# Optimization experiments

Measured on AMD Instinct MI355X. Metric: run time of the kernel, lower is better.

The kernel has to match this reference:

```python
import jax, jax.numpy as jnp
from jax import lax
import numpy as np

N_E = 1024
E_DIM = 512
BETA = 0.25


def setup_inputs() -> dict:
    key = jax.random.key(0)
    k1, k2 = jax.random.split(key)
    z = jax.random.normal(k1, (16, 4096, E_DIM), dtype=jnp.float32)
    # torch init: uniform(-1/n_e, 1/n_e)
    codebook = jax.random.uniform(k2, (N_E, E_DIM), dtype=jnp.float32,
                                  minval=-1.0 / N_E, maxval=1.0 / N_E)
    return {"z": z, "codebook": codebook}


def reference(z, codebook):
    zf = z.reshape(-1, z.shape[-1])                      # (N, e_dim)
    # squared-distance matrix: ||z||^2 + ||e||^2 - 2 z e^T  -> (N, n_e)
    d = (jnp.sum(zf * zf, axis=1, keepdims=True)
         + jnp.sum(codebook * codebook, axis=1)
         - 2.0 * (zf @ codebook.T))
    idx = jnp.argmin(d, axis=1)                          # (N,)
    z_q = codebook[idx].reshape(z.shape)                 # (B, S, e_dim)
    loss = (jnp.mean((z_q - lax.stop_gradient(z)) ** 2)
            + BETA * jnp.mean((lax.stop_gradient(z_q) - z) ** 2))
    # straight-through estimator
    z_q_st = z + lax.stop_gradient(z_q - z)
    # perplexity of code usage (mean of one-hot == normalized counts)
    counts = jnp.zeros((codebook.shape[0],), dtype=z.dtype).at[idx].add(1.0)
    e_mean = counts / idx.shape[0]
    perplexity = jnp.exp(-jnp.sum(e_mean * jnp.log(e_mean + 1e-10)))
    return (loss, z_q_st, idx, perplexity)
```

## Files before the change

kernel.cpp:

```cpp
#include <hip/hip_runtime.h>
#include <hip/hip_bf16.h>

#define N_ROWS 65536
#define EDIM   512
#define NCODES 1024

#define WS_LOSS   0
#define WS_COUNTS 1
#define WS_ENORM  1025
#define WS_ZNORM  2049
#define WS_AMBCNT (2049 + 65536)
#define WS_WINNER (WS_AMBCNT + 1)
#define WS_AMBLST (WS_WINNER + 65536)
#define AMB_CAP   32768
#define WS_E2_OFF (1u << 20)
#define WS_FAST_BYTES (3u * 1024u * 1024u + 4096u)

#define AMB_EPS 1.6e-4f

typedef short short8 __attribute__((ext_vector_type(8)));
typedef float f32x4  __attribute__((ext_vector_type(4)));

#define AS1C(p) ((const __attribute__((address_space(1))) void*)(p))
#define AS3(p)  ((__attribute__((address_space(3))) void*)(p))

static __device__ __forceinline__ unsigned short f2bf(float f) {
    unsigned u = __float_as_uint(f);
    u += 0x7FFFu + ((u >> 16) & 1u);
    return (unsigned short)(u >> 16);
}
static __device__ __forceinline__ float bf2f(unsigned short h) {
    return __uint_as_float(((unsigned)h) << 16);
}

__global__ __launch_bounds__(256) void vq_prep(const float* __restrict__ cb,
                                               float* __restrict__ ws) {
    int j = blockIdx.x;
    int tid = threadIdx.x;
    float2 v = *(const float2*)&cb[(size_t)j * EDIM + tid * 2];
    float s = v.x * v.x + v.y * v.y;
    #pragma unroll
    for (int off = 32; off > 0; off >>= 1) s += __shfl_down(s, off);
    __shared__ float ls[4];
    int wave = tid >> 6, lane = tid & 63;
    if (lane == 0) ls[wave] = s;
    __syncthreads();
    if (tid == 0) {
        ws[WS_ENORM + j] = ls[0] + ls[1] + ls[2] + ls[3];
        ws[WS_COUNTS + j] = 0.0f;
        if (j == 0) {
            ws[WS_LOSS] = 0.0f;
            ((int*)ws)[WS_AMBCNT] = 0;
        }
    }
}

__global__ __launch_bounds__(256) void vq_znorm(const float* __restrict__ z,
                                                float* __restrict__ ws) {
    int tid  = threadIdx.x;
    int lrow = tid >> 5;
    int c    = tid & 31;
    long row = (long)blockIdx.x * 8 + lrow;
    const float* p = z + row * EDIM + (c >> 3) * 128 + (c & 7);
    float r = p[0] * p[0];
    #pragma unroll
    for (int i = 1; i < 16; ++i) {
        float v = p[i * 8];
        r += v * v;
    }
    r += __shfl_xor(r, 1);
    r += __shfl_xor(r, 2);
    r += __shfl_xor(r, 4);
    r += __shfl_xor(r, 8);
    r += __shfl_xor(r, 16);
    if (c == 0) ws[WS_ZNORM + row] = r;
}

__global__ __launch_bounds__(256) void vq_convz(const float* __restrict__ z,
                                                unsigned short* __restrict__ z2) {
    const int tid = threadIdx.x;
    const int p = blockIdx.x;
    const long row0 = (long)p * 128;
    const int row = tid >> 1, half = tid & 1;
    for (int kc = 0; kc < 16; ++kc) {
        const float* src = z + (row0 + row) * EDIM + kc * 32 + half * 16;
        float f[16];
        #pragma unroll
        for (int q = 0; q < 4; ++q) {
            float4 v = ((const float4*)src)[q];
            f[q*4+0] = v.x; f[q*4+1] = v.y; f[q*4+2] = v.z; f[q*4+3] = v.w;
        }
        unsigned hi[8], lo[8];
        #pragma unroll
        for (int q = 0; q < 8; ++q) {
            unsigned short h0 = f2bf(f[2*q]);
            unsigned short h1 = f2bf(f[2*q+1]);
            unsigned short l0 = f2bf(f[2*q]   - bf2f(h0));
            unsigned short l1 = f2bf(f[2*q+1] - bf2f(h1));
            hi[q] = (unsigned)h0 | ((unsigned)h1 << 16);
            lo[q] = (unsigned)l0 | ((unsigned)l1 << 16);
        }
        size_t base = ((size_t)(p * 16 + kc) * 2) * 4096;
        unsigned* dhi = (unsigned*)(z2 + base        + row * 32 + half * 16);
        unsigned* dlo = (unsigned*)(z2 + base + 4096 + row * 32 + half * 16);
        ((uint4*)dhi)[0] = make_uint4(hi[0], hi[1], hi[2], hi[3]);
        ((uint4*)dhi)[1] = make_uint4(hi[4], hi[5], hi[6], hi[7]);
        ((uint4*)dlo)[0] = make_uint4(lo[0], lo[1], lo[2], lo[3]);
        ((uint4*)dlo)[1] = make_uint4(lo[4], lo[5], lo[6], lo[7]);
    }
}

__global__ __launch_bounds__(256) void vq_convcb(const float* __restrict__ cb,
                                                 unsigned short* __restrict__ e2) {
    const int tid = threadIdx.x;
    const int cc = blockIdx.x;
    const int row = tid >> 1, half = tid & 1;
    for (int kc = 0; kc < 16; ++kc) {
        const float* src = cb + (size_t)(cc * 128 + row) * EDIM + kc * 32 + half * 16;
        float f[16];
        #pragma unroll
        for (int q = 0; q < 4; ++q) {
            float4 v = ((const float4*)src)[q];
            f[q*4+0] = v.x; f[q*4+1] = v.y; f[q*4+2] = v.z; f[q*4+3] = v.w;
        }
        unsigned hi[8], lo[8];
        #pragma unroll
        for (int q = 0; q < 8; ++q) {
            unsigned short h0 = f2bf(f[2*q]);
            unsigned short h1 = f2bf(f[2*q+1]);
            unsigned short l0 = f2bf(f[2*q]   - bf2f(h0));
            unsigned short l1 = f2bf(f[2*q+1] - bf2f(h1));
            hi[q] = (unsigned)h0 | ((unsigned)h1 << 16);
            lo[q] = (unsigned)l0 | ((unsigned)l1 << 16);
        }
        size_t base = ((size_t)(cc * 16 + kc) * 2) * 4096;
        unsigned* dhi = (unsigned*)(e2 + base        + row * 32 + half * 16);
        unsigned* dlo = (unsigned*)(e2 + base + 4096 + row * 32 + half * 16);
        ((uint4*)dhi)[0] = make_uint4(hi[0], hi[1], hi[2], hi[3]);
        ((uint4*)dhi)[1] = make_uint4(hi[4], hi[5], hi[6], hi[7]);
        ((uint4*)dlo)[0] = make_uint4(lo[0], lo[1], lo[2], lo[3]);
        ((uint4*)dlo)[1] = make_uint4(lo[4], lo[5], lo[6], lo[7]);
    }
}

__device__ __forceinline__ void stage_chunk(const char* src, char* dst, int goff0,
                                            int wb) {
    __builtin_amdgcn_global_load_lds(AS1C(src + goff0),        AS3(dst + wb),        16, 0, 0);
    __builtin_amdgcn_global_load_lds(AS1C(src + goff0 + 4096), AS3(dst + 8192 + wb), 16, 0, 0);
}

__device__ __forceinline__ void stage_step(const char* zb, const char* eb, char* buf,
                                           int goff0, int wb) {
    stage_chunk(zb,              buf,         goff0, wb);
    stage_chunk(zb + 16 * 16384, buf + 16384, goff0, wb);
    stage_chunk(eb,              buf + 32768, goff0, wb);
    stage_chunk(eb + 16 * 16384, buf + 49152, goff0, wb);
}

__global__ __launch_bounds__(512, 2) void vq_mfma(const unsigned short* __restrict__ z2,
                                                  const unsigned short* __restrict__ e2,
                                                  const float* __restrict__ ws,
                                                  int* __restrict__ winner,
                                                  int* __restrict__ amb_count,
                                                  int* __restrict__ amb_list) {
    __shared__ __attribute__((aligned(16))) char sb[2][65536];
    __shared__ float enorm_lds[NCODES];
    __shared__ float fv1[2][256];
    __shared__ float fv2[2][256];
    __shared__ int   fc1[2][256];

    const int tid  = threadIdx.x;
    const int lane = tid & 63, w = tid >> 6;
    const int wr   = (w & 3) * 64;
    const int wcg  = w >> 2;
    const int wc   = wcg * 128;
    const int ml = lane & 15, kg = lane >> 4;
    const long row0 = (long)blockIdx.x * 256;

    const int t3 = tid >> 3;
    const int sl = (tid & 7) ^ (t3 & 7);
    const int goff0 = t3 * 64 + (sl & 3) * 16 + (sl >> 2) * 8192;
    const int wb = w << 10;

    const int xr = ml & 7;
    const int o0 = (kg ^ xr) * 16;
    const int o1 = ((4 + kg) ^ xr) * 16;
    const int za = (wr + ml) * 128;
    const int ea = 32768 + (wc + ml) * 128;

    enorm_lds[tid]       = ws[WS_ENORM + tid];
    enorm_lds[tid + 512] = ws[WS_ENORM + tid + 512];

    float v1[16], v2[16];
    int   c1[16];
    #pragma unroll
    for (int i = 0; i < 16; ++i) { v1[i] = INFINITY; v2[i] = INFINITY; c1[i] = 0; }

    const char* z2b = (const char*)z2 + (size_t)blockIdx.x * 2 * 16 * 16384;
    const char* e2b = (const char*)e2;

    f32x4 acc[4][8];
    #pragma unroll
    for (int rt = 0; rt < 4; ++rt)
        #pragma unroll
        for (int ct = 0; ct < 8; ++ct)
            acc[rt][ct] = (f32x4){0.f, 0.f, 0.f, 0.f};

    stage_step(z2b, e2b, sb[0], goff0, wb);
    __syncthreads();

    int cur = 0;
    #pragma unroll 2
    for (int s = 0; s < 64; ++s) {
        if (s + 1 < 64) {
            const int s2 = s + 1, cc2 = s2 >> 4, kc2 = s2 & 15;
            stage_step(z2b + (size_t)kc2 * 16384,
                       e2b + (size_t)(cc2 * 32 + kc2) * 16384,
                       sb[cur ^ 1], goff0, wb);
        }
        const char* bz = sb[cur];
        short8 a[4][2];
        #pragma unroll
        for (int rt = 0; rt < 4; ++rt) {
            a[rt][0] = *(const short8*)(bz + za + rt * 2048 + o0);
            a[rt][1] = *(const short8*)(bz + za + rt * 2048 + o1);
        }
        #pragma unroll
        for (int ct = 0; ct < 8; ++ct) {
            short8 b0 = *(const short8*)(bz + ea + ct * 2048 + o0);
            short8 b1 = *(const short8*)(bz + ea + ct * 2048 + o1);
            #pragma unroll
            for (int rt = 0; rt < 4; ++rt) {
                acc[rt][ct] = __builtin_amdgcn_mfma_f32_16x16x32_bf16(a[rt][0], b0, acc[rt][ct], 0, 0, 0);
                acc[rt][ct] = __builtin_amdgcn_mfma_f32_16x16x32_bf16(a[rt][0], b1, acc[rt][ct], 0, 0, 0);
                acc[rt][ct] = __builtin_amdgcn_mfma_f32_16x16x32_bf16(a[rt][1], b0, acc[rt][ct], 0, 0, 0);
            }
        }
        asm volatile("s_waitcnt vmcnt(0)" ::: "memory");
        __builtin_amdgcn_s_barrier();
        asm volatile("" ::: "memory");
        cur ^= 1;

        if ((s & 15) == 15) {
            const int cc = s >> 4;
            #pragma unroll
            for (int ct = 0; ct < 8; ++ct) {
                const int code = cc * 256 + wc + ct * 16 + ml;
                const float en = enorm_lds[code];
                #pragma unroll
                for (int rt = 0; rt < 4; ++rt)
                    #pragma unroll
                    for (int reg = 0; reg < 4; ++reg) {
                        float d = fmaf(-2.0f, acc[rt][ct][reg], en);
                        int i = rt * 4 + reg;
                        bool lt1 = d < v1[i];
                        bool lt2 = d < v2[i];
                        v2[i] = lt1 ? v1[i] : (lt2 ? d : v2[i]);
                        v1[i] = lt1 ? d : v1[i];
                        c1[i] = lt1 ? code : c1[i];
                    }
            }
            #pragma unroll
            for (int rt = 0; rt < 4; ++rt)
                #pragma unroll
                for (int ct = 0; ct < 8; ++ct)
                    acc[rt][ct] = (f32x4){0.f, 0.f, 0.f, 0.f};
        }
    }

    #pragma unroll
    for (int i = 0; i < 16; ++i) {
        #pragma unroll
        for (int off = 1; off < 16; off <<= 1) {
            float ov1 = __shfl_xor(v1[i], off);
            int   oc1 = __shfl_xor(c1[i], off);
            float ov2 = __shfl_xor(v2[i], off);
            bool take = (ov1 < v1[i]) || (ov1 == v1[i] && oc1 < c1[i]);
            float nv2 = take ? fminf(v1[i], ov2) : fminf(v2[i], ov1);
            v1[i] = take ? ov1 : v1[i];
            c1[i] = take ? oc1 : c1[i];
            v2[i] = nv2;
        }
    }
    __syncthreads();
    if (ml == 0) {
        #pragma unroll
        for (int i = 0; i < 16; ++i) {
            int row = wr + (i >> 2) * 16 + kg * 4 + (i & 3);
            fv1[wcg][row] = v1[i];
            fv2[wcg][row] = v2[i];
            fc1[wcg][row] = c1[i];
        }
    }
    __syncthreads();
    if (tid < 256) {
        float a1 = fv1[0][tid], a2 = fv2[0][tid];
        int   ac = fc1[0][tid];
        float b1 = fv1[1][tid], b2 = fv2[1][tid];
        int   bc = fc1[1][tid];
        bool take = (b1 < a1) || (b1 == a1 && bc < ac);
        float V1 = take ? b1 : a1;
        int   C1 = take ? bc : ac;
        float V2 = take ? fminf(a1, b2) : fminf(a2, b1);
        winner[row0 + tid] = C1;
        if (V2 - V1 < AMB_EPS) {
            int p = atomicAdd(amb_count, 1);
            if (p < AMB_CAP) amb_list[p] = (int)(row0 + tid);
        }
    }
}

#define RB 8
#define ZSR 9
__global__ __launch_bounds__(256) void vq_recheck(const float* __restrict__ z,
                                                  const float* __restrict__ cb,
                                                  const float* __restrict__ ws,
                                                  int* __restrict__ winner,
                                                  const int* __restrict__ amb_count,
                                                  const int* __restrict__ amb_list) {
    __shared__ float zs[EDIM * ZSR];
    __shared__ float wred_d[4];
    __shared__ int   wred_i[4];
    const int tid = threadIdx.x;
    const int lane = tid & 63, wv = tid >> 6;
    const float* __restrict__ enorm = ws + WS_ENORM;

    int n = *amb_count;
    bool overflow = (n > AMB_CAP);
    if (overflow) n = N_ROWS;
    int nIter = (n + RB - 1) / RB;

    const float* ec[4];
    float en4[4];
    #pragma unroll
    for (int c = 0; c < 4; ++c) {
        ec[c]  = cb + (size_t)(tid + 256 * c) * EDIM;
        en4[c] = enorm[tid + 256 * c];
    }

    for (int ii = blockIdx.x; ii < nIter; ii += gridDim.x) {
        int rows[RB];
        #pragma unroll
        for (int j = 0; j < RB; ++j) {
            int idx = ii * RB + j;
            if (idx >= n) idx = n - 1;
            rows[j] = overflow ? idx : amb_list[idx];
        }
        __syncthreads();
        #pragma unroll
        for (int j = 0; j < RB; ++j) {
            float2 v = *(const float2*)&z[(long)rows[j] * EDIM + tid * 2];
            zs[(tid * 2 + 0) * ZSR + j] = v.x;
            zs[(tid * 2 + 1) * ZSR + j] = v.y;
        }
        __syncthreads();

        float acc[RB][4];
        #pragma unroll
        for (int r = 0; r < RB; ++r)
            #pragma unroll
            for (int c = 0; c < 4; ++c) acc[r][c] = 0.0f;

        for (int k0 = 0; k0 < EDIM; k0 += 32) {
            float ain[RB][4];
            #pragma unroll
            for (int r = 0; r < RB; ++r)
                #pragma unroll
                for (int c = 0; c < 4; ++c) ain[r][c] = 0.0f;
            #pragma unroll
            for (int ks = 0; ks < 32; ks += 8) {
                float er[4][8];
                #pragma unroll
                for (int c = 0; c < 4; ++c) {
                    float4 a = *(const float4*)&ec[c][k0 + ks];
                    float4 b = *(const float4*)&ec[c][k0 + ks + 4];
                    er[c][0]=a.x; er[c][1]=a.y; er[c][2]=a.z; er[c][3]=a.w;
                    er[c][4]=b.x; er[c][5]=b.y; er[c][6]=b.z; er[c][7]=b.w;
                }
                #pragma unroll
                for (int kk = 0; kk < 8; ++kk) {
                    const float* zp = &zs[(k0 + ks + kk) * ZSR];
                    float4 z0 = *(const float4*)zp;
                    float4 z1 = *(const float4*)(zp + 4);
                    float zr[RB] = {z0.x, z0.y, z0.z, z0.w, z1.x, z1.y, z1.z, z1.w};
                    #pragma unroll
                    for (int r = 0; r < RB; ++r)
                        #pragma unroll
                        for (int c = 0; c < 4; ++c)
                            ain[r][c] = fmaf(zr[r], er[c][kk], ain[r][c]);
                }
            }
            #pragma unroll
            for (int r = 0; r < RB; ++r)
                #pragma unroll
                for (int c = 0; c < 4; ++c) acc[r][c] += ain[r][c];
        }

        #pragma unroll
        for (int r = 0; r < RB; ++r) {
            float zn = ws[WS_ZNORM + rows[r]];
            float bd = INFINITY;
            int   bc = 0;
            #pragma unroll
            for (int c = 0; c < 4; ++c) {
                float t = zn + en4[c];
                float d = t - 2.0f * acc[r][c];
                if (d < bd) { bd = d; bc = tid + 256 * c; }
            }
            #pragma unroll
            for (int off = 1; off < 64; off <<= 1) {
                float od = __shfl_xor(bd, off);
                int   oi = __shfl_xor(bc, off);
                if (od < bd || (od == bd && oi < bc)) { bd = od; bc = oi; }
            }
            if (lane == 0) { wred_d[wv] = bd; wred_i[wv] = bc; }
            __syncthreads();
            if (tid == 0) {
                float fd = wred_d[0]; int fi = wred_i[0];
                #pragma unroll
                for (int t2 = 1; t2 < 4; ++t2) {
                    if (wred_d[t2] < fd || (wred_d[t2] == fd && wred_i[t2] < fi)) {
                        fd = wred_d[t2]; fi = wred_i[t2];
                    }
                }
                winner[rows[r]] = fi;
            }
            __syncthreads();
        }
    }
}

__global__ __launch_bounds__(256) void vq_emit(const float* __restrict__ z,
                                               const float* __restrict__ cb,
                                               const int* __restrict__ winner,
                                               float* __restrict__ ws,
                                               float* __restrict__ out_zq,
                                               float* __restrict__ out_idx) {
    __shared__ float lred[4];
    const int tid = threadIdx.x;
    const long row0 = (long)blockIdx.x * 128;
    if (tid < 128) {
        int wi = winner[row0 + tid];
        out_idx[row0 + tid] = (float)wi;
        atomicAdd(&ws[WS_COUNTS + wi], 1.0f);
    }
    float lsum = 0.0f;
    for (int r = 0; r < 128; ++r) {
        int wv = winner[row0 + r];
        float2 e  = *(const float2*)&cb[(size_t)wv * EDIM + tid * 2];
        float2 zz = *(const float2*)&z[(row0 + r) * EDIM + tid * 2];
        float d0 = e.x - zz.x, d1 = e.y - zz.y;
        float2 o; o.x = zz.x + d0; o.y = zz.y + d1;
        *(float2*)&out_zq[(row0 + r) * EDIM + tid * 2] = o;
        lsum = fmaf(d0, d0, fmaf(d1, d1, lsum));
    }
    #pragma unroll
    for (int off = 32; off > 0; off >>= 1) lsum += __shfl_down(lsum, off);
    int wave = tid >> 6, lane = tid & 63;
    if (lane == 0) lred[wave] = lsum;
    __syncthreads();
    if (tid == 0) atomicAdd(&ws[WS_LOSS], lred[0] + lred[1] + lred[2] + lred[3]);
}

__global__ __launch_bounds__(1024) void vq_final(const float* __restrict__ ws,
                                                 float* __restrict__ out,
                                                 long off_perp) {
    int tid = threadIdx.x;
    float c = ws[WS_COUNTS + tid] * (1.0f / (float)N_ROWS);
    float t = c * logf(c + 1e-10f);
    #pragma unroll
    for (int off = 32; off > 0; off >>= 1) t += __shfl_down(t, off);
    __shared__ float ls[16];
    int wave = tid >> 6, lane = tid & 63;
    if (lane == 0) ls[wave] = t;
    __syncthreads();
    if (tid == 0) {
        float h = 0.0f;
        #pragma unroll
        for (int i = 0; i < 16; ++i) h += ls[i];
        out[off_perp] = expf(-h);
        out[0] = ws[WS_LOSS] * 1.25f / (float)((long)N_ROWS * EDIM);
    }
}

#define ROWS_PER_BLOCK 128
#define CODE_CHUNK     64
#define KCHUNK         32
#define ZSTRIDE        132
#define ESTRIDE        68

__global__ __launch_bounds__(256) void vq_main_fb(const float* __restrict__ z,
                                                  const float* __restrict__ cb,
                                                  float* __restrict__ ws,
                                                  float* __restrict__ out_zq,
                                                  float* __restrict__ out_idx) {
    __shared__ float zt[KCHUNK * ZSTRIDE];
    __shared__ float et[KCHUNK * ESTRIDE];
    __shared__ float red_d[ROWS_PER_BLOCK * 8];
    __shared__ int   red_i[ROWS_PER_BLOCK * 8];
    __shared__ int   winner[ROWS_PER_BLOCK];
    __shared__ float lred[4];

    const int tid = threadIdx.x;
    const int tx = tid & 7;
    const int ty = tid >> 3;
    const long row0 = (long)blockIdx.x * ROWS_PER_BLOCK;
    const float* __restrict__ enorm = ws + WS_ENORM;
    const float* __restrict__ znorm = ws + WS_ZNORM;

    float zn[4];
    #pragma unroll
    for (int i = 0; i < 4; ++i) zn[i] = znorm[row0 + ty * 4 + i];

    float best[4];
    int   bidx[4];
    #pragma unroll
    for (int i = 0; i < 4; ++i) { best[i] = INFINITY; bidx[i] = 0; }

    const int kq    = (tid & 7) * 4;
    const int rbase = tid >> 3;

    for (int c = 0; c < NCODES; c += CODE_CHUNK) {
        float acc[4][8];
        #pragma unroll
        for (int i = 0; i < 4; ++i)
            #pragma unroll
            for (int j = 0; j < 8; ++j) acc[i][j] = 0.0f;

        for (int k0 = 0; k0 < EDIM; k0 += KCHUNK) {
            __syncthreads();
            #pragma unroll
            for (int it = 0; it < 4; ++it) {
                int r = rbase + it * 32;
                float4 v = *(const float4*)&z[(row0 + r) * EDIM + k0 + kq];
                zt[(kq + 0) * ZSTRIDE + r] = v.x;
                zt[(kq + 1) * ZSTRIDE + r] = v.y;
                zt[(kq + 2) * ZSTRIDE + r] = v.z;
                zt[(kq + 3) * ZSTRIDE + r] = v.w;
            }
            #pragma unroll
            for (int it = 0; it < 2; ++it) {
                int e = rbase + it * 32;
                float4 v = *(const float4*)&cb[(size_t)(c + e) * EDIM + k0 + kq];
                et[(kq + 0) * ESTRIDE + e] = v.x;
                et[(kq + 1) * ESTRIDE + e] = v.y;
                et[(kq + 2) * ESTRIDE + e] = v.z;
                et[(kq + 3) * ESTRIDE + e] = v.w;
            }
            __syncthreads();
            float ain[4][8];
            #pragma unroll
            for (int i = 0; i < 4; ++i)
                #pragma unroll
                for (int j = 0; j < 8; ++j) ain[i][j] = 0.0f;
            #pragma unroll
            for (int kk = 0; kk < KCHUNK; ++kk) {
                float4 zv = *(const float4*)&zt[kk * ZSTRIDE + ty * 4];
                float4 e0 = *(const float4*)&et[kk * ESTRIDE + tx * 8];
                float4 e1 = *(const float4*)&et[kk * ESTRIDE + tx * 8 + 4];
                float za[4] = {zv.x, zv.y, zv.z, zv.w};
                float ea[8] = {e0.x, e0.y, e0.z, e0.w, e1.x, e1.y, e1.z, e1.w};
                #pragma unroll
                for (int i = 0; i < 4; ++i)
                    #pragma unroll
                    for (int j = 0; j < 8; ++j)
                        ain[i][j] = fmaf(za[i], ea[j], ain[i][j]);
            }
            #pragma unroll
            for (int i = 0; i < 4; ++i)
                #pragma unroll
                for (int j = 0; j < 8; ++j) acc[i][j] += ain[i][j];
        }
        #pragma unroll
        for (int j = 0; j < 8; ++j) {
            int code = c + tx * 8 + j;
            float en = enorm[code];
            #pragma unroll
            for (int i = 0; i < 4; ++i) {
                float t = zn[i] + en;
                float d = t - 2.0f * acc[i][j];
                if (d < best[i]) { best[i] = d; bidx[i] = code; }
            }
        }
    }

    __syncthreads();
    #pragma unroll
    for (int i = 0; i < 4; ++i) {
        red_d[(ty * 4 + i) * 8 + tx] = best[i];
        red_i[(ty * 4 + i) * 8 + tx] = bidx[i];
    }
    __syncthreads();
    if (tid < ROWS_PER_BLOCK) {
        float bd = red_d[tid * 8];
        int   bi = red_i[tid * 8];
        #pragma unroll
        for (int t = 1; t < 8; ++t) {
            float dv = red_d[tid * 8 + t];
            int   iv = red_i[tid * 8 + t];
            if (dv < bd || (dv == bd && iv < bi)) { bd = dv; bi = iv; }
        }
        winner[tid] = bi;
        out_idx[row0 + tid] = (float)bi;
        atomicAdd(&ws[WS_COUNTS + bi], 1.0f);
    }
    __syncthreads();

    float lsum = 0.0f;
    for (int r = 0; r < ROWS_PER_BLOCK; ++r) {
        int w = winner[r];
        float2 e  = *(const float2*)&cb[(size_t)w * EDIM + tid * 2];
        float2 zz = *(const float2*)&z[(row0 + r) * EDIM + tid * 2];
        float d0 = e.x - zz.x, d1 = e.y - zz.y;
        float2 o; o.x = zz.x + d0; o.y = zz.y + d1;
        *(float2*)&out_zq[(row0 + r) * EDIM + tid * 2] = o;
        lsum = fmaf(d0, d0, fmaf(d1, d1, lsum));
    }
    #pragma unroll
    for (int off = 32; off > 0; off >>= 1) lsum += __shfl_down(lsum, off);
    int wave = tid >> 6, lane = tid & 63;
    if (lane == 0) lred[wave] = lsum;
    __syncthreads();
    if (tid == 0) atomicAdd(&ws[WS_LOSS], lred[0] + lred[1] + lred[2] + lred[3]);
}

extern "C" void kernel_launch(void* const* d_in, const int* in_sizes, int n_in,
                              void* d_out, int out_size, void* d_ws, size_t ws_size,
                              hipStream_t stream) {
    const float* z  = (const float*)d_in[0];
    const float* cb = (const float*)d_in[1];
    float* out = (float*)d_out;
    float* ws  = (float*)d_ws;

    float* out_zq  = out + 1;
    float* out_idx = out + 1 + (long)N_ROWS * EDIM;
    long   off_perp = 1 + (long)N_ROWS * EDIM + N_ROWS;

    hipLaunchKernelGGL(vq_prep, dim3(NCODES), dim3(256), 0, stream, cb, ws);
    hipLaunchKernelGGL(vq_znorm, dim3(N_ROWS / 8), dim3(256), 0, stream, z, ws);

    if (ws_size >= (size_t)WS_FAST_BYTES) {
        unsigned short* z2 = (unsigned short*)(out + 4);
        unsigned short* e2 = (unsigned short*)((char*)d_ws + WS_E2_OFF);
        int* winner    = ((int*)ws) + WS_WINNER;
        int* amb_count = ((int*)ws) + WS_AMBCNT;
        int* amb_list  = ((int*)ws) + WS_AMBLST;

        hipLaunchKernelGGL(vq_convz, dim3(N_ROWS / 128), dim3(256), 0, stream, z, z2);
        hipLaunchKernelGGL(vq_convcb, dim3(8), dim3(256), 0, stream, cb, e2);
        hipLaunchKernelGGL(vq_mfma, dim3(N_ROWS / 256), dim3(512), 0, stream,
                           z2, e2, ws, winner, amb_count, amb_list);
        hipLaunchKernelGGL(vq_recheck, dim3(1024), dim3(256), 0, stream,
                           z, cb, ws, winner, amb_count, amb_list);
        hipLaunchKernelGGL(vq_emit, dim3(N_ROWS / 128), dim3(256), 0, stream,
                           z, cb, winner, ws, out_zq, out_idx);
    } else {
        hipLaunchKernelGGL(vq_main_fb, dim3(N_ROWS / 128), dim3(256), 0, stream,
                           z, cb, ws, out_zq, out_idx);
    }
    hipLaunchKernelGGL(vq_final, dim3(1), dim3(1024), 0, stream, ws, out, off_perp);
}
```

Measured before the change: 680.0 us.

## Add two-step-ahead L2 prefetch into scrap LDS and widen emit loads

The MFMA kernel now issues extra global_load_lds requests for the data of step s+2 into a throwaway LDS scrap buffer. The goal is to warm L2/MALL before the real staging load, hiding global latency. The emit kernel caches winner indices in shared memory and has each wave process whole rows with float4 loads and stores instead of float2 per thread. The prefetch doubles global load traffic issued per step, and the scrap writes add LDS pressure. Because it sits after the waitcnt, it may also stall the next iteration's vmcnt wait.

```diff
diff --git a/kernel.cpp b/kernel.cpp
--- a/kernel.cpp
+++ b/kernel.cpp
@@ -157,6 +157,18 @@
     stage_chunk(eb + 16 * 16384, buf + 49152, goff0, wb);
 }
 
+__device__ __forceinline__ void pf_step_lds(const char* zb, const char* eb,
+                                            char* scrap, int t16, int wb) {
+    __builtin_amdgcn_global_load_lds(AS1C(zb + t16),                     AS3(scrap + wb), 16, 0, 0);
+    __builtin_amdgcn_global_load_lds(AS1C(zb + t16 + 8192),              AS3(scrap + wb), 16, 0, 0);
+    __builtin_amdgcn_global_load_lds(AS1C(zb + 16 * 16384 + t16),        AS3(scrap + wb), 16, 0, 0);
+    __builtin_amdgcn_global_load_lds(AS1C(zb + 16 * 16384 + t16 + 8192), AS3(scrap + wb), 16, 0, 0);
+    __builtin_amdgcn_global_load_lds(AS1C(eb + t16),                     AS3(scrap + wb), 16, 0, 0);
+    __builtin_amdgcn_global_load_lds(AS1C(eb + t16 + 8192),              AS3(scrap + wb), 16, 0, 0);
+    __builtin_amdgcn_global_load_lds(AS1C(eb + 16 * 16384 + t16),        AS3(scrap + wb), 16, 0, 0);
+    __builtin_amdgcn_global_load_lds(AS1C(eb + 16 * 16384 + t16 + 8192), AS3(scrap + wb), 16, 0, 0);
+}
+
 __global__ __launch_bounds__(512, 2) void vq_mfma(const unsigned short* __restrict__ z2,
                                                   const unsigned short* __restrict__ e2,
                                                   const float* __restrict__ ws,
@@ -164,6 +176,7 @@
                                                   int* __restrict__ amb_count,
                                                   int* __restrict__ amb_list) {
     __shared__ __attribute__((aligned(16))) char sb[2][65536];
+    __shared__ __attribute__((aligned(16))) char pfscrap[8192];
     __shared__ float enorm_lds[NCODES];
     __shared__ float fv1[2][256];
     __shared__ float fv2[2][256];
@@ -176,6 +189,7 @@
     const int wc   = wcg * 128;
     const int ml = lane & 15, kg = lane >> 4;
     const long row0 = (long)blockIdx.x * 256;
+    const int t16 = tid * 16;
 
     const int t3 = tid >> 3;
     const int sl = (tid & 7) ^ (t3 & 7);
@@ -207,6 +221,7 @@
             acc[rt][ct] = (f32x4){0.f, 0.f, 0.f, 0.f};
 
     stage_step(z2b, e2b, sb[0], goff0, wb);
+    pf_step_lds(z2b + 16384, e2b + 16384, pfscrap, t16, wb);
     __syncthreads();
 
     int cur = 0;
@@ -237,6 +252,12 @@
             }
         }
         asm volatile("s_waitcnt vmcnt(0)" ::: "memory");
+        if (s + 2 < 64) {
+            const int s3 = s + 2, cc3 = s3 >> 4, kc3 = s3 & 15;
+            pf_step_lds(z2b + (size_t)kc3 * 16384,
+                        e2b + (size_t)(cc3 * 32 + kc3) * 16384,
+                        pfscrap, t16, wb);
+        }
         __builtin_amdgcn_s_barrier();
         asm volatile("" ::: "memory");
         cur ^= 1;
@@ -436,28 +457,40 @@
                                                float* __restrict__ ws,
                                                float* __restrict__ out_zq,
                                                float* __restrict__ out_idx) {
+    __shared__ int   wsh[128];
     __shared__ float lred[4];
     const int tid = threadIdx.x;
+    const int lane = tid & 63, wv = tid >> 6;
     const long row0 = (long)blockIdx.x * 128;
     if (tid < 128) {
         int wi = winner[row0 + tid];
+        wsh[tid] = wi;
         out_idx[row0 + tid] = (float)wi;
         atomicAdd(&ws[WS_COUNTS + wi], 1.0f);
     }
+    __syncthreads();
     float lsum = 0.0f;
-    for (int r = 0; r < 128; ++r) {
-        int wv = winner[row0 + r];
-        float2 e  = *(const float2*)&cb[(size_t)wv * EDIM + tid * 2];
-        float2 zz = *(const float2*)&z[(row0 + r) * EDIM + tid * 2];
-        float d0 = e.x - zz.x, d1 = e.y - zz.y;
-        float2 o; o.x = zz.x + d0; o.y = zz.y + d1;
-        *(float2*)&out_zq[(row0 + r) * EDIM + tid * 2] = o;
-        lsum = fmaf(d0, d0, fmaf(d1, d1, lsum));
+    for (int it = 0; it < 32; ++it) {
+        const int r = it * 4 + wv;
+        const int wi = wsh[r];
+        const float4* ep = (const float4*)(cb + (size_t)wi * EDIM);
+        const float4* zp = (const float4*)(z + (row0 + r) * EDIM);
+        float4*       op = (float4*)(out_zq + (row0 + r) * EDIM);
+        #pragma unroll
+        for (int h = 0; h < 2; ++h) {
+            float4 e  = ep[lane + h * 64];
+            float4 zz = zp[lane + h * 64];
+            float d0 = e.x - zz.x, d1 = e.y - zz.y;
+            float d2 = e.z - zz.z, d3 = e.w - zz.w;
+            float4 o;
+            o.x = zz.x + d0; o.y = zz.y + d1; o.z = zz.z + d2; o.w = zz.w + d3;
+            op[lane + h * 64] = o;
+            lsum = fmaf(d0, d0, fmaf(d1, d1, fmaf(d2, d2, fmaf(d3, d3, lsum))));
+        }
     }
     #pragma unroll
     for (int off = 32; off > 0; off >>= 1) lsum += __shfl_down(lsum, off);
-    int wave = tid >> 6, lane = tid & 63;
-    if (lane == 0) lred[wave] = lsum;
+    if (lane == 0) lred[wv] = lsum;
     __syncthreads();
     if (tid == 0) atomicAdd(&ws[WS_LOSS], lred[0] + lred[1] + lred[2] + lred[3]);
 }
```

After: 696.1 us. 1.02x slower.
